# Kernel optimization log

Measured on AMD Instinct MI355X. Metric: run time of the kernel, lower is better.

The kernel has to match this reference:

```python
import jax, jax.numpy as jnp
import numpy as np

BN_EPS = 1e-3  # keras BatchNormalization default


def _bn(x, gamma, beta, mean, var):
    # inference-mode batchnorm over channel (last) axis
    return (x - mean) * (gamma * jax.lax.rsqrt(var + BN_EPS)) + beta


def _rel_pos_idx(n):
    # replicate calc_rel_pos: pos (n*n, 2); rel = pos[None]-pos[:,None] + n-1
    ii, jj = np.meshgrid(np.arange(n), np.arange(n), indexing='ij')
    pos = np.stack([ii.reshape(-1), jj.reshape(-1)], axis=-1)  # (n*n, 2)
    rel = pos[None, :, :] - pos[:, None, :] + (n - 1)          # (n*n, n*n, 2)
    return jnp.asarray(rel, dtype=jnp.int32)


def setup_inputs() -> dict:
    key = jax.random.key(0)
    ks = jax.random.split(key, 13)
    b, hh, ww, c = 4, 16, 16, 1024
    heads, dim_k, dim_u, dim_out = 4, 256, 1, 1024
    dim_v = dim_out // heads  # 256 == dim_k (required by the original reshape)
    n = hh
    rel_len = 2 * n - 1
    inp = {
        'x': jax.random.normal(ks[0], (b, hh, ww, c), jnp.float32),
        'Wq': jax.random.normal(ks[1], (c, dim_k * heads), jnp.float32) * 0.02,
        'Wk': jax.random.normal(ks[2], (c, dim_k * dim_u), jnp.float32) * 0.02,
        'Wv': jax.random.normal(ks[3], (c, dim_v * dim_u), jnp.float32) * 0.02,
        'q_gamma': jax.random.normal(ks[4], (dim_k * heads,), jnp.float32),
        'q_beta': jax.random.normal(ks[5], (dim_k * heads,), jnp.float32),
        'q_mean': jax.random.normal(ks[6], (dim_k * heads,), jnp.float32),
        'q_var': jax.random.uniform(ks[7], (dim_k * heads,), jnp.float32, 0.5, 1.5),
        'v_gamma': jax.random.normal(ks[8], (dim_v * dim_u,), jnp.float32),
        'v_beta': jax.random.normal(ks[9], (dim_v * dim_u,), jnp.float32),
        'v_mean': jax.random.normal(ks[10], (dim_v * dim_u,), jnp.float32),
        'v_var': jax.random.uniform(ks[11], (dim_v * dim_u,), jnp.float32, 0.5, 1.5),
        'rel_pos_emb': jax.random.normal(ks[12], (rel_len, rel_len, dim_k, dim_u), jnp.float32) * 0.05,
    }
    return inp


def reference(x, Wq, Wk, Wv, q_gamma, q_beta, q_mean, q_var,
              v_gamma, v_beta, v_mean, v_var, rel_pos_emb):
    b, hh, ww, c = x.shape
    heads, dim_u = 4, 1
    dim_k = rel_pos_emb.shape[2]
    dim_v = Wv.shape[1] // dim_u
    m = hh * ww

    # 1x1 conv projections (no bias)
    q = jnp.einsum('bhwc,cd->bhwd', x, Wq)
    k = jnp.einsum('bhwc,cd->bhwd', x, Wk)
    v = jnp.einsum('bhwc,cd->bhwd', x, Wv)

    q = _bn(q, q_gamma, q_beta, q_mean, q_var)
    v = _bn(v, v_gamma, v_beta, v_mean, v_var)

    # faithful TF row-major reshapes (note: mixes spatial/channel exactly as original)
    q = q.reshape(b, heads, dim_v, m)   # (b, h, k, n)
    k = k.reshape(b, dim_u, dim_v, m)   # (b, u, k, m)
    v = v.reshape(b, dim_u, dim_v, m)   # (b, u, v, m)

    k = jax.nn.softmax(k, axis=-1)

    Lc = jnp.einsum('bukm,buvm->bkv', k, v)
    Yc = jnp.einsum('bhkn,bkv->bnhv', q, Lc)

    rel_pos = _rel_pos_idx(hh)  # (m, m, 2) int32 constants
    rel = rel_pos_emb[rel_pos[..., 0], rel_pos[..., 1]]  # (m, m, k, u)
    Lp = jnp.einsum('nmku,buvm->bnkv', rel, v)
    Yp = jnp.einsum('bhkn,bnkv->bnhv', q, Lp)

    Y = Yc + Yp  # (b, n, h, v)
    return Y.reshape(b, hh, ww, heads * dim_v)
```

## Files before the change

kernel.cpp:

```cpp
#include <hip/hip_runtime.h>


typedef __bf16 bf16;
typedef __attribute__((ext_vector_type(8))) __bf16 bf16x8;
typedef __attribute__((ext_vector_type(4))) float f32x4;

__device__ __forceinline__ bf16x8 ld8(const bf16* p) {
    return *reinterpret_cast<const bf16x8*>(p);
}

__global__ __launch_bounds__(256) void prep(
    const float* __restrict__ x, const float* __restrict__ Wq,
    const float* __restrict__ Wk, const float* __restrict__ Wv,
    const float* __restrict__ rpe, bf16* __restrict__ xb,
    bf16* __restrict__ WqT, bf16* __restrict__ WkT, bf16* __restrict__ WvT,
    bf16* __restrict__ rpeb) {
    __shared__ float tile[32][33];
    const int bid = blockIdx.x, tid = threadIdx.x;
    const float* W = nullptr;
    bf16* WT = nullptr;
    int ldw = 0, ci = 0, di = 0;
    if (bid < 1024) {
        W = Wq; WT = WqT; ldw = 1024; ci = bid >> 5; di = bid & 31;
    } else if (bid < 1280) {
        const int t2 = bid - 1024;
        W = Wk; WT = WkT; ldw = 256; ci = t2 >> 3; di = t2 & 7;
    } else if (bid < 1536) {
        const int t2 = bid - 1280;
        W = Wv; WT = WvT; ldw = 256; ci = t2 >> 3; di = t2 & 7;
    }
    if (W) {
        const int r = tid >> 3, c4 = (tid & 7) * 4;
        const float4 v =
            *reinterpret_cast<const float4*>(&W[(ci * 32 + r) * ldw + di * 32 + c4]);
        tile[r][c4 + 0] = v.x;
        tile[r][c4 + 1] = v.y;
        tile[r][c4 + 2] = v.z;
        tile[r][c4 + 3] = v.w;
        __syncthreads();
        bf16 o[4] = {(bf16)tile[c4 + 0][r], (bf16)tile[c4 + 1][r],
                     (bf16)tile[c4 + 2][r], (bf16)tile[c4 + 3][r]};
        *reinterpret_cast<uint2*>(&WT[(di * 32 + r) * 1024 + ci * 32 + c4]) =
            *reinterpret_cast<uint2*>(o);
        return;
    }
    if (bid < 1792) {
        const int base = (bid - 1536) * 1024 + tid;
        const float4* xs = reinterpret_cast<const float4*>(x);
#pragma unroll
        for (int j = 0; j < 4; ++j) {
            const float4 v = xs[base + j * 256];
            bf16 o[4] = {(bf16)v.x, (bf16)v.y, (bf16)v.z, (bf16)v.w};
            *reinterpret_cast<uint2*>(&xb[(base + j * 256) * 4]) =
                *reinterpret_cast<uint2*>(o);
        }
        return;
    }
    {
        const int base = (bid - 1792) * 1024 + tid;
        const float4* rs = reinterpret_cast<const float4*>(rpe);
#pragma unroll
        for (int j = 0; j < 4; ++j) {
            const int idx = base + j * 256;
            if (idx < 61504) {
                const float4 v = rs[idx];
                bf16 o[4] = {(bf16)v.x, (bf16)v.y, (bf16)v.z, (bf16)v.w};
                *reinterpret_cast<uint2*>(&rpeb[idx * 4]) =
                    *reinterpret_cast<uint2*>(o);
            }
        }
    }
}

template <int PA, int PB>
__device__ __forceinline__ void kpass128(const bf16* __restrict__ Ap, int offA,
                                         const bf16* __restrict__ Bp,
                                         bf16* __restrict__ Al, bf16* __restrict__ Bl,
                                         f32x4 (&acc)[2], int m0, int n0,
                                         int nsteps) {
    const int tid = threadIdx.x;
    const int w = tid >> 6, l = tid & 63;
    const int sr = tid >> 4;
    const int sg = tid & 15;
    const int wrow = (w & 1) * 16, wcol = (w >> 1) * 32;
    const int fr = l & 15, fg = l >> 4;
    const int fx7 = fr & 7;
    const int st = sr * 128 + ((sg ^ (sr & 7)) << 3);
    const bf16* asrc0 = Ap + (m0 + sr) * PA + offA + sg * 8;
    const bf16* asrc1 = asrc0 + 16 * PA;
    const bf16* bsrc0 = Bp + (n0 + sr) * PB + sg * 8;
    const bf16* bsrc1 = bsrc0 + 16 * PB;
    const bf16* bsrc2 = bsrc0 + 32 * PB;
    const bf16* bsrc3 = bsrc0 + 48 * PB;

    bf16x8 a0 = ld8(asrc0), a1 = ld8(asrc1);
    bf16x8 b0 = ld8(bsrc0), b1 = ld8(bsrc1), b2 = ld8(bsrc2), b3 = ld8(bsrc3);
    for (int kt = 0; kt < nsteps; ++kt) {
        __syncthreads();
        *reinterpret_cast<bf16x8*>(&Al[st]) = a0;
        *reinterpret_cast<bf16x8*>(&Al[st + 2048]) = a1;
        *reinterpret_cast<bf16x8*>(&Bl[st]) = b0;
        *reinterpret_cast<bf16x8*>(&Bl[st + 2048]) = b1;
        *reinterpret_cast<bf16x8*>(&Bl[st + 4096]) = b2;
        *reinterpret_cast<bf16x8*>(&Bl[st + 6144]) = b3;
        __syncthreads();
        if (kt + 1 < nsteps) {
            const int k0 = (kt + 1) * 128;
            a0 = ld8(asrc0 + k0);
            a1 = ld8(asrc1 + k0);
            b0 = ld8(bsrc0 + k0);
            b1 = ld8(bsrc1 + k0);
            b2 = ld8(bsrc2 + k0);
            b3 = ld8(bsrc3 + k0);
        }
#pragma unroll
        for (int ks = 0; ks < 4; ++ks) {
            const int eo = ((ks * 4 + fg) ^ fx7) << 3;
            const bf16x8 af = ld8(&Al[(wrow + fr) * 128 + eo]);
            const bf16x8 bg0 = ld8(&Bl[(wcol + fr) * 128 + eo]);
            const bf16x8 bg1 = ld8(&Bl[(wcol + 16 + fr) * 128 + eo]);
            acc[0] = __builtin_amdgcn_mfma_f32_16x16x32_bf16(af, bg0, acc[0], 0, 0, 0);
            acc[1] = __builtin_amdgcn_mfma_f32_16x16x32_bf16(af, bg1, acc[1], 0, 0, 0);
        }
    }
}

__global__ __launch_bounds__(256) void proj_all(
    const bf16* __restrict__ xb, const bf16* __restrict__ WqT,
    const bf16* __restrict__ WkT, const bf16* __restrict__ WvT,
    const float* __restrict__ qg, const float* __restrict__ qb,
    const float* __restrict__ qm, const float* __restrict__ qv,
    const float* __restrict__ vg, const float* __restrict__ vb,
    const float* __restrict__ vm, const float* __restrict__ vvar,
    bf16* __restrict__ Q2, float* __restrict__ kn, bf16* __restrict__ vbn) {
    const int z = blockIdx.z;
    const int m0 = blockIdx.y * 32;
    const int tid = threadIdx.x;
    const int w = tid >> 6, l = tid & 63;
    int n0, mode;
    const bf16* Bg;
    if (z < 4) { mode = 0; Bg = WqT; n0 = (z * 4 + blockIdx.x) * 64; }
    else if (z == 4) { mode = 1; Bg = WkT; n0 = blockIdx.x * 64; }
    else { mode = 2; Bg = WvT; n0 = blockIdx.x * 64; }
    __shared__ __align__(16) bf16 Al[4096];
    __shared__ __align__(16) bf16 Bl[8192];
    f32x4 acc[2] = {};
    kpass128<1024, 1024>(xb, 0, Bg, Al, Bl, acc, m0, n0, 8);

    const int wrow = (w & 1) * 16, wcol = (w >> 1) * 32;
    const int drow = (l >> 4) * 4, dcol = l & 15;
#pragma unroll
    for (int ns = 0; ns < 2; ++ns) {
        const int gc = n0 + wcol + ns * 16 + dcol;
        float scale = 1.f, shift = 0.f;
        if (mode == 0) {
            scale = qg[gc] * rsqrtf(qv[gc] + 1e-3f);
            shift = qb[gc] - qm[gc] * scale;
        } else if (mode == 2) {
            scale = vg[gc] * rsqrtf(vvar[gc] + 1e-3f);
            shift = vb[gc] - vm[gc] * scale;
        }
#pragma unroll
        for (int r = 0; r < 4; ++r) {
            const int gr = m0 + wrow + drow + r;
            const float val = acc[ns][r] * scale + shift;
            if (mode == 0) {
                const int bh = gr >> 6;
                const int kk = (gr & 63) * 4 + (gc >> 8);
                Q2[bh * 65536 + (gc & 255) * 256 + kk] = (bf16)val;
            } else if (mode == 1) {
                kn[gr * 256 + gc] = val;
            } else {
                vbn[gr * 256 + gc] = (bf16)val;
            }
        }
    }
}

__global__ __launch_bounds__(256) void lc_s(
    const float* __restrict__ kn, const bf16* __restrict__ vbn,
    const bf16* __restrict__ rpeb, const bf16* __restrict__ Q2,
    bf16* __restrict__ LcT, bf16* __restrict__ S) {
    __shared__ __align__(16) bf16 smem[20480];
    const int tid = threadIdx.x;
    const int w = tid >> 6, l = tid & 63;
    const int fr = l & 15, fk = (l >> 4) * 8;
    const int fx = (fr & 7) << 3;

    if (blockIdx.y < 16) {
        const int b = blockIdx.y >> 2;
        const int m0v = (blockIdx.y & 3) * 64;
        const int n0k = blockIdx.x * 64;
        bf16* Bfull = smem;
        bf16* Al = smem + 16384;

        const float* knb = kn + (b * 256 + n0k) * 256;
        const int row = tid >> 2, cq = (tid & 3) * 4;
        const float* src = knb + row * 256;
        float mx = -3.4e38f;
#pragma unroll
        for (int i = 0; i < 16; ++i) {
            const float4 v = *reinterpret_cast<const float4*>(&src[cq + i * 16]);
            mx = fmaxf(fmaxf(fmaxf(v.x, v.y), fmaxf(v.z, v.w)), mx);
        }
        mx = fmaxf(mx, __shfl_xor(mx, 1));
        mx = fmaxf(mx, __shfl_xor(mx, 2));
        float sum = 0.f;
#pragma unroll
        for (int i = 0; i < 16; ++i) {
            const float4 v = *reinterpret_cast<const float4*>(&src[cq + i * 16]);
            sum += expf(v.x - mx) + expf(v.y - mx) + expf(v.z - mx) + expf(v.w - mx);
        }
        sum += __shfl_xor(sum, 1);
        sum += __shfl_xor(sum, 2);
        const float inv = 1.f / sum;
#pragma unroll
        for (int i = 0; i < 16; ++i) {
            const int col = cq + i * 16;
            const float4 v = *reinterpret_cast<const float4*>(&src[col]);
            bf16 o[4] = {(bf16)(expf(v.x - mx) * inv), (bf16)(expf(v.y - mx) * inv),
                         (bf16)(expf(v.z - mx) * inv), (bf16)(expf(v.w - mx) * inv)};
            const int elem =
                row * 256 + ((((col >> 3) ^ (row & 7)) << 3) | (col & 7));
            *reinterpret_cast<uint2*>(&Bfull[elem]) = *reinterpret_cast<uint2*>(o);
        }

        const int sr0 = tid >> 3, sg = tid & 7;
        const int st0 = sr0 * 64 + ((sg ^ (sr0 & 7)) << 3);
        const int st1 = (sr0 + 32) * 64 + ((sg ^ (sr0 & 7)) << 3);
        const int wr = (w >> 1) * 32, wc = (w & 1) * 32;
        const bf16* va0 = vbn + (b * 256 + m0v + sr0) * 256 + sg * 8;
        const bf16* va1 = va0 + 32 * 256;
        bf16x8 a0 = ld8(va0), a1 = ld8(va1);
        f32x4 acc[2][2] = {};
        for (int kt = 0; kt < 4; ++kt) {
            __syncthreads();
            *reinterpret_cast<bf16x8*>(&Al[st0]) = a0;
            *reinterpret_cast<bf16x8*>(&Al[st1]) = a1;
            __syncthreads();
            if (kt + 1 < 4) {
                a0 = ld8(va0 + (kt + 1) * 64);
                a1 = ld8(va1 + (kt + 1) * 64);
            }
#pragma unroll
            for (int ks = 0; ks < 2; ++ks) {
                const int eoA = (ks * 32 + fk) ^ fx;
                const int eoB = (kt * 64 + ks * 32 + fk) ^ fx;
                const bf16x8 af0 = ld8(&Al[(wr + fr) * 64 + eoA]);
                const bf16x8 af1 = ld8(&Al[(wr + 16 + fr) * 64 + eoA]);
                const bf16x8 bg0 = ld8(&Bfull[(wc + fr) * 256 + eoB]);
                const bf16x8 bg1 = ld8(&Bfull[(wc + 16 + fr) * 256 + eoB]);
                acc[0][0] = __builtin_amdgcn_mfma_f32_16x16x32_bf16(af0, bg0, acc[0][0], 0, 0, 0);
                acc[0][1] = __builtin_amdgcn_mfma_f32_16x16x32_bf16(af0, bg1, acc[0][1], 0, 0, 0);
                acc[1][0] = __builtin_amdgcn_mfma_f32_16x16x32_bf16(af1, bg0, acc[1][0], 0, 0, 0);
                acc[1][1] = __builtin_amdgcn_mfma_f32_16x16x32_bf16(af1, bg1, acc[1][1], 0, 0, 0);
            }
        }
        const int drow = (l >> 4) * 4, dcol = l & 15;
#pragma unroll
        for (int ms = 0; ms < 2; ++ms)
#pragma unroll
            for (int ns = 0; ns < 2; ++ns)
#pragma unroll
                for (int r = 0; r < 4; ++r)
                    LcT[b * 65536 + (m0v + wr + ms * 16 + drow + r) * 256 + n0k +
                        wc + ns * 16 + dcol] = (bf16)acc[ms][ns][r];
        return;
    }

    const int n = blockIdx.y - 16;
    const int m0 = blockIdx.x * 64;
    const int in_ = n >> 4, jn = n & 15;
    bf16* Als = smem;
    bf16* Bls = smem + 16384;
#pragma unroll
    for (int i = 0; i < 2; ++i) {
        const int slot = tid + i * 256;
        const int row = slot >> 5, g = slot & 31;
        *reinterpret_cast<bf16x8*>(&Bls[row * 256 + ((g ^ (row & 7)) << 3)]) =
            ld8(Q2 + row * 65536 + n * 256 + g * 8);
    }
#pragma unroll
    for (int i = 0; i < 8; ++i) {
        const int slot = tid + i * 256;
        const int row = slot >> 5, g = slot & 31;
        const int m = m0 + row;
        const int ridx = ((m >> 4) - in_ + 15) * 31 + ((m & 15) - jn + 15);
        *reinterpret_cast<bf16x8*>(&Als[row * 256 + ((g ^ (row & 7)) << 3)]) =
            ld8(rpeb + ridx * 256 + g * 8);
    }
    __syncthreads();
    f32x4 acc = {};
#pragma unroll
    for (int ks = 0; ks < 8; ++ks) {
        const int eo = (ks * 32 + fk) ^ fx;
        const bf16x8 af = ld8(&Als[(w * 16 + fr) * 256 + eo]);
        const bf16x8 bg = ld8(&Bls[fr * 256 + eo]);
        acc = __builtin_amdgcn_mfma_f32_16x16x32_bf16(af, bg, acc, 0, 0, 0);
    }
    const int drow = (l >> 4) * 4, bh = l & 15;
#pragma unroll
    for (int r = 0; r < 4; ++r) {
        const int m = m0 + w * 16 + drow + r;
        S[n * 4096 + bh * 256 + m] = (bf16)acc[r];
    }
}

__global__ __launch_bounds__(256) void yfinal(const bf16* __restrict__ Q2,
                                              const bf16* __restrict__ LcT,
                                              float* __restrict__ out,
                                              const bf16* __restrict__ S,
                                              const bf16* __restrict__ vbn) {
    const int tid = threadIdx.x;
    const int w = tid >> 6, l = tid & 63;
    const int m0 = blockIdx.y * 32, n0 = blockIdx.x * 64;
    const int z = blockIdx.z;
    __shared__ __align__(16) bf16 Al[4096];
    __shared__ __align__(16) bf16 Bl[8192];
    f32x4 acc[2] = {};
    kpass128<256, 256>(Q2 + z * 65536, 0, LcT + (z >> 2) * 65536, Al, Bl, acc, m0,
                       n0, 2);
    kpass128<4096, 256>(S, z * 256, vbn + (z >> 2) * 65536, Al, Bl, acc, m0, n0, 2);

    const int wrow = (w & 1) * 16, wcol = (w >> 1) * 32;
    const int drow = (l >> 4) * 4, dcol = l & 15;
#pragma unroll
    for (int ns = 0; ns < 2; ++ns)
#pragma unroll
        for (int r = 0; r < 4; ++r)
            out[(z >> 2) * 262144 + (m0 + wrow + drow + r) * 1024 +
                (z & 3) * 256 + n0 + wcol + ns * 16 + dcol] = acc[ns][r];
}

extern "C" void kernel_launch(void* const* d_in, const int* in_sizes, int n_in,
                              void* d_out, int out_size, void* d_ws, size_t ws_size,
                              hipStream_t stream) {
    const float* x = (const float*)d_in[0];
    const float* Wq = (const float*)d_in[1];
    const float* Wk = (const float*)d_in[2];
    const float* Wv = (const float*)d_in[3];
    const float* qg = (const float*)d_in[4];
    const float* qb = (const float*)d_in[5];
    const float* qm = (const float*)d_in[6];
    const float* qv = (const float*)d_in[7];
    const float* vg = (const float*)d_in[8];
    const float* vb = (const float*)d_in[9];
    const float* vm = (const float*)d_in[10];
    const float* vvar = (const float*)d_in[11];
    const float* rpe = (const float*)d_in[12];
    float* out = (float*)d_out;

    char* wsb = (char*)d_ws;
    bf16* xb = (bf16*)(wsb);
    bf16* WqT = (bf16*)(wsb + 0x200000u);
    bf16* WkT = (bf16*)(wsb + 0x400000u);
    bf16* WvT = (bf16*)(wsb + 0x480000u);
    bf16* rpeb = (bf16*)(wsb + 0x500000u);
    bf16* Q2 = (bf16*)(wsb + 0x580000u);
    bf16* vbn = (bf16*)(wsb + 0x800000u);
    bf16* LcT = (bf16*)(wsb + 0x880000u);
    bf16* S = (bf16*)(wsb + 0x900000u);
    float* kn = (float*)(wsb + 0xB00000u);

    const dim3 blk(256);
    prep<<<1853, blk, 0, stream>>>(x, Wq, Wk, Wv, rpe, xb, WqT, WkT, WvT, rpeb);
    proj_all<<<dim3(4, 32, 6), blk, 0, stream>>>(xb, WqT, WkT, WvT, qg, qb, qm, qv,
                                                 vg, vb, vm, vvar, Q2, kn, vbn);
    lc_s<<<dim3(4, 272), blk, 0, stream>>>(kn, vbn, rpeb, Q2, LcT, S);
    yfinal<<<dim3(4, 8, 16), blk, 0, stream>>>(Q2, LcT, out, S, vbn);
}
```

Before: 39.92 us.

## Fuse projection, Lc/S and final stages into persistent kernel with grid barriers

Result: slower. 138.1 us (+245.9%).

```diff
diff --git a/kernel.cpp b/kernel.cpp
--- a/kernel.cpp
+++ b/kernel.cpp
@@ -5,8 +5,21 @@
 typedef __attribute__((ext_vector_type(8))) __bf16 bf16x8;
 typedef __attribute__((ext_vector_type(4))) float f32x4;
 
+#define NBLK 512u
+
 __device__ __forceinline__ bf16x8 ld8(const bf16* p) {
     return *reinterpret_cast<const bf16x8*>(p);
+}
+
+__device__ __forceinline__ void gridbar(unsigned int* cnt) {
+    __syncthreads();
+    if (threadIdx.x == 0) {
+        __threadfence();
+        atomicAdd(cnt, 1u);
+        while (atomicAdd(cnt, 0u) < NBLK) __builtin_amdgcn_s_sleep(8);
+        __threadfence();
+    }
+    __syncthreads();
 }
 
 __global__ __launch_bounds__(256) void prep(
@@ -14,9 +27,10 @@
     const float* __restrict__ Wk, const float* __restrict__ Wv,
     const float* __restrict__ rpe, bf16* __restrict__ xb,
     bf16* __restrict__ WqT, bf16* __restrict__ WkT, bf16* __restrict__ WvT,
-    bf16* __restrict__ rpeb) {
+    bf16* __restrict__ rpeb, unsigned int* cnt) {
     __shared__ float tile[32][33];
     const int bid = blockIdx.x, tid = threadIdx.x;
+    if (bid == 0 && tid < 2) cnt[tid * 16] = 0u;
     const float* W = nullptr;
     bf16* WT = nullptr;
     int ldw = 0, ci = 0, di = 0;
@@ -125,211 +139,213 @@
     }
 }
 
-__global__ __launch_bounds__(256) void proj_all(
+__global__ __launch_bounds__(256, 2) void fused(
     const bf16* __restrict__ xb, const bf16* __restrict__ WqT,
     const bf16* __restrict__ WkT, const bf16* __restrict__ WvT,
     const float* __restrict__ qg, const float* __restrict__ qb,
     const float* __restrict__ qm, const float* __restrict__ qv,
     const float* __restrict__ vg, const float* __restrict__ vb,
     const float* __restrict__ vm, const float* __restrict__ vvar,
-    bf16* __restrict__ Q2, float* __restrict__ kn, bf16* __restrict__ vbn) {
-    const int z = blockIdx.z;
-    const int m0 = blockIdx.y * 32;
+    bf16* __restrict__ Q2, float* __restrict__ kn, bf16* __restrict__ vbn,
+    const bf16* __restrict__ rpeb, bf16* __restrict__ LcT, bf16* __restrict__ S,
+    float* __restrict__ out, unsigned int* cnt) {
+    __shared__ __align__(16) char smem_raw[40960];
+    const int bid = blockIdx.x;
     const int tid = threadIdx.x;
     const int w = tid >> 6, l = tid & 63;
-    int n0, mode;
-    const bf16* Bg;
-    if (z < 4) { mode = 0; Bg = WqT; n0 = (z * 4 + blockIdx.x) * 64; }
-    else if (z == 4) { mode = 1; Bg = WkT; n0 = blockIdx.x * 64; }
-    else { mode = 2; Bg = WvT; n0 = blockIdx.x * 64; }
-    __shared__ __align__(16) bf16 Al[4096];
-    __shared__ __align__(16) bf16 Bl[8192];
-    f32x4 acc[2] = {};
-    kpass128<1024, 1024>(xb, 0, Bg, Al, Bl, acc, m0, n0, 8);
-
-    const int wrow = (w & 1) * 16, wcol = (w >> 1) * 32;
-    const int drow = (l >> 4) * 4, dcol = l & 15;
-#pragma unroll
-    for (int ns = 0; ns < 2; ++ns) {
-        const int gc = n0 + wcol + ns * 16 + dcol;
-        float scale = 1.f, shift = 0.f;
-        if (mode == 0) {
-            scale = qg[gc] * rsqrtf(qv[gc] + 1e-3f);
-            shift = qb[gc] - qm[gc] * scale;
-        } else if (mode == 2) {
-            scale = vg[gc] * rsqrtf(vvar[gc] + 1e-3f);
-            shift = vb[gc] - vm[gc] * scale;
-        }
-#pragma unroll
-        for (int r = 0; r < 4; ++r) {
-            const int gr = m0 + wrow + drow + r;
-            const float val = acc[ns][r] * scale + shift;
+
+    for (int j = bid; j < 768; j += NBLK) {
+        bf16* Al = (bf16*)smem_raw;
+        bf16* Bl = (bf16*)(smem_raw + 8192);
+        const int z = j >> 7;
+        const int m0 = ((j >> 2) & 31) * 32;
+        const int bx = j & 3;
+        int n0, mode;
+        const bf16* Bg;
+        if (z < 4) { mode = 0; Bg = WqT; n0 = (z * 4 + bx) * 64; }
+        else if (z == 4) { mode = 1; Bg = WkT; n0 = bx * 64; }
+        else { mode = 2; Bg = WvT; n0 = bx * 64; }
+        f32x4 acc[2] = {};
+        kpass128<1024, 1024>(xb, 0, Bg, Al, Bl, acc, m0, n0, 8);
+
+        const int wrow = (w & 1) * 16, wcol = (w >> 1) * 32;
+        const int drow = (l >> 4) * 4, dcol = l & 15;
+#pragma unroll
+        for (int ns = 0; ns < 2; ++ns) {
+            const int gc = n0 + wcol + ns * 16 + dcol;
+            float scale = 1.f, shift = 0.f;
             if (mode == 0) {
-                const int bh = gr >> 6;
-                const int kk = (gr & 63) * 4 + (gc >> 8);
-                Q2[bh * 65536 + (gc & 255) * 256 + kk] = (bf16)val;
-            } else if (mode == 1) {
-                kn[gr * 256 + gc] = val;
-            } else {
-                vbn[gr * 256 + gc] = (bf16)val;
-            }
-        }
-    }
-}
-
-__global__ __launch_bounds__(256) void lc_s(
-    const float* __restrict__ kn, const bf16* __restrict__ vbn,
-    const bf16* __restrict__ rpeb, const bf16* __restrict__ Q2,
-    bf16* __restrict__ LcT, bf16* __restrict__ S) {
-    __shared__ __align__(16) bf16 smem[20480];
-    const int tid = threadIdx.x;
-    const int w = tid >> 6, l = tid & 63;
-    const int fr = l & 15, fk = (l >> 4) * 8;
-    const int fx = (fr & 7) << 3;
-
-    if (blockIdx.y < 16) {
-        const int b = blockIdx.y >> 2;
-        const int m0v = (blockIdx.y & 3) * 64;
-        const int n0k = blockIdx.x * 64;
-        bf16* Bfull = smem;
-        bf16* Al = smem + 16384;
-
-        const float* knb = kn + (b * 256 + n0k) * 256;
-        const int row = tid >> 2, cq = (tid & 3) * 4;
-        const float* src = knb + row * 256;
-        float mx = -3.4e38f;
-#pragma unroll
-        for (int i = 0; i < 16; ++i) {
-            const float4 v = *reinterpret_cast<const float4*>(&src[cq + i * 16]);
-            mx = fmaxf(fmaxf(fmaxf(v.x, v.y), fmaxf(v.z, v.w)), mx);
-        }
-        mx = fmaxf(mx, __shfl_xor(mx, 1));
-        mx = fmaxf(mx, __shfl_xor(mx, 2));
-        float sum = 0.f;
-#pragma unroll
-        for (int i = 0; i < 16; ++i) {
-            const float4 v = *reinterpret_cast<const float4*>(&src[cq + i * 16]);
-            sum += expf(v.x - mx) + expf(v.y - mx) + expf(v.z - mx) + expf(v.w - mx);
-        }
-        sum += __shfl_xor(sum, 1);
-        sum += __shfl_xor(sum, 2);
-        const float inv = 1.f / sum;
-#pragma unroll
-        for (int i = 0; i < 16; ++i) {
-            const int col = cq + i * 16;
-            const float4 v = *reinterpret_cast<const float4*>(&src[col]);
-            bf16 o[4] = {(bf16)(expf(v.x - mx) * inv), (bf16)(expf(v.y - mx) * inv),
-                         (bf16)(expf(v.z - mx) * inv), (bf16)(expf(v.w - mx) * inv)};
-            const int elem =
-                row * 256 + ((((col >> 3) ^ (row & 7)) << 3) | (col & 7));
-            *reinterpret_cast<uint2*>(&Bfull[elem]) = *reinterpret_cast<uint2*>(o);
-        }
-
-        const int sr0 = tid >> 3, sg = tid & 7;
-        const int st0 = sr0 * 64 + ((sg ^ (sr0 & 7)) << 3);
-        const int st1 = (sr0 + 32) * 64 + ((sg ^ (sr0 & 7)) << 3);
-        const int wr = (w >> 1) * 32, wc = (w & 1) * 32;
-        const bf16* va0 = vbn + (b * 256 + m0v + sr0) * 256 + sg * 8;
-        const bf16* va1 = va0 + 32 * 256;
-        bf16x8 a0 = ld8(va0), a1 = ld8(va1);
-        f32x4 acc[2][2] = {};
-        for (int kt = 0; kt < 4; ++kt) {
+                scale = qg[gc] * rsqrtf(qv[gc] + 1e-3f);
+                shift = qb[gc] - qm[gc] * scale;
+            } else if (mode == 2) {
+                scale = vg[gc] * rsqrtf(vvar[gc] + 1e-3f);
+                shift = vb[gc] - vm[gc] * scale;
+            }
+#pragma unroll
+            for (int r = 0; r < 4; ++r) {
+                const int gr = m0 + wrow + drow + r;
+                const float val = acc[ns][r] * scale + shift;
+                if (mode == 0) {
+                    const int bh = gr >> 6;
+                    const int kk = (gr & 63) * 4 + (gc >> 8);
+                    Q2[bh * 65536 + (gc & 255) * 256 + kk] = (bf16)val;
+                } else if (mode == 1) {
+                    kn[gr * 256 + gc] = val;
+                } else {
+                    vbn[gr * 256 + gc] = (bf16)val;
+                }
+            }
+        }
+        __syncthreads();
+    }
+    gridbar(cnt);
+
+    for (int j = bid; j < 1088; j += NBLK) {
+        bf16* smem = (bf16*)smem_raw;
+        const int jx = j & 3, jy = j >> 2;
+        const int fr = l & 15, fk = (l >> 4) * 8;
+        const int fx = (fr & 7) << 3;
+
+        if (jy < 16) {
+            const int b = jy >> 2;
+            const int m0v = (jy & 3) * 64;
+            const int n0k = jx * 64;
+            bf16* Bfull = smem;
+            bf16* Al = smem + 16384;
+
+            const float* knb = kn + (b * 256 + n0k) * 256;
+            const int row = tid >> 2, cq = (tid & 3) * 4;
+            const float* src = knb + row * 256;
+            float mx = -3.4e38f;
+#pragma unroll
+            for (int i = 0; i < 16; ++i) {
+                const float4 v = *reinterpret_cast<const float4*>(&src[cq + i * 16]);
+                mx = fmaxf(fmaxf(fmaxf(v.x, v.y), fmaxf(v.z, v.w)), mx);
+            }
+            mx = fmaxf(mx, __shfl_xor(mx, 1));
+            mx = fmaxf(mx, __shfl_xor(mx, 2));
+            float sum = 0.f;
+#pragma unroll
+            for (int i = 0; i < 16; ++i) {
+                const float4 v = *reinterpret_cast<const float4*>(&src[cq + i * 16]);
+                sum += expf(v.x - mx) + expf(v.y - mx) + expf(v.z - mx) + expf(v.w - mx);
+            }
+            sum += __shfl_xor(sum, 1);
+            sum += __shfl_xor(sum, 2);
+            const float inv = 1.f / sum;
+#pragma unroll
+            for (int i = 0; i < 16; ++i) {
+                const int col = cq + i * 16;
+                const float4 v = *reinterpret_cast<const float4*>(&src[col]);
+                bf16 o[4] = {(bf16)(expf(v.x - mx) * inv), (bf16)(expf(v.y - mx) * inv),
+                             (bf16)(expf(v.z - mx) * inv), (bf16)(expf(v.w - mx) * inv)};
+                const int elem =
+                    row * 256 + ((((col >> 3) ^ (row & 7)) << 3) | (col & 7));
+                *reinterpret_cast<uint2*>(&Bfull[elem]) = *reinterpret_cast<uint2*>(o);
+            }
+
+            const int sr0 = tid >> 3, sg = tid & 7;
+            const int st0 = sr0 * 64 + ((sg ^ (sr0 & 7)) << 3);
+            const int st1 = (sr0 + 32) * 64 + ((sg ^ (sr0 & 7)) << 3);
+            const int wr = (w >> 1) * 32, wc = (w & 1) * 32;
+            const bf16* va0 = vbn + (b * 256 + m0v + sr0) * 256 + sg * 8;
+            const bf16* va1 = va0 + 32 * 256;
+            bf16x8 a0 = ld8(va0), a1 = ld8(va1);
+            f32x4 acc[2][2] = {};
+            for (int kt = 0; kt < 4; ++kt) {
+                __syncthreads();
+                *reinterpret_cast<bf16x8*>(&Al[st0]) = a0;
+                *reinterpret_cast<bf16x8*>(&Al[st1]) = a1;
+                __syncthreads();
+                if (kt + 1 < 4) {
+                    a0 = ld8(va0 + (kt + 1) * 64);
+                    a1 = ld8(va1 + (kt + 1) * 64);
+                }
+#pragma unroll
+                for (int ks = 0; ks < 2; ++ks) {
+                    const int eoA = (ks * 32 + fk) ^ fx;
+                    const int eoB = (kt * 64 + ks * 32 + fk) ^ fx;
+                    const bf16x8 af0 = ld8(&Al[(wr + fr) * 64 + eoA]);
+                    const bf16x8 af1 = ld8(&Al[(wr + 16 + fr) * 64 + eoA]);
+                    const bf16x8 bg0 = ld8(&Bfull[(wc + fr) * 256 + eoB]);
+                    const bf16x8 bg1 = ld8(&Bfull[(wc + 16 + fr) * 256 + eoB]);
+                    acc[0][0] = __builtin_amdgcn_mfma_f32_16x16x32_bf16(af0, bg0, acc[0][0], 0, 0, 0);
+                    acc[0][1] = __builtin_amdgcn_mfma_f32_16x16x32_bf16(af0, bg1, acc[0][1], 0, 0, 0);
+                    acc[1][0] = __builtin_amdgcn_mfma_f32_16x16x32_bf16(af1, bg0, acc[1][0], 0, 0, 0);
+                    acc[1][1] = __builtin_amdgcn_mfma_f32_16x16x32_bf16(af1, bg1, acc[1][1], 0, 0, 0);
+                }
+            }
+            const int drow = (l >> 4) * 4, dcol = l & 15;
+#pragma unroll
+            for (int ms = 0; ms < 2; ++ms)
+#pragma unroll
+                for (int ns = 0; ns < 2; ++ns)
+#pragma unroll
+                    for (int r = 0; r < 4; ++r)
+                        LcT[b * 65536 + (m0v + wr + ms * 16 + drow + r) * 256 + n0k +
+                            wc + ns * 16 + dcol] = (bf16)acc[ms][ns][r];
+        } else {
+            const int n = jy - 16;
+            const int m0 = jx * 64;
+            const int in_ = n >> 4, jn = n & 15;
+            bf16* Als = smem;
+            bf16* Bls = smem + 16384;
+#pragma unroll
+            for (int i = 0; i < 2; ++i) {
+                const int slot = tid + i * 256;
+                const int row = slot >> 5, g = slot & 31;
+                *reinterpret_cast<bf16x8*>(&Bls[row * 256 + ((g ^ (row & 7)) << 3)]) =
+                    ld8(Q2 + row * 65536 + n * 256 + g * 8);
+            }
+#pragma unroll
+            for (int i = 0; i < 8; ++i) {
+                const int slot = tid + i * 256;
+                const int row = slot >> 5, g = slot & 31;
+                const int m = m0 + row;
+                const int ridx = ((m >> 4) - in_ + 15) * 31 + ((m & 15) - jn + 15);
+                *reinterpret_cast<bf16x8*>(&Als[row * 256 + ((g ^ (row & 7)) << 3)]) =
+                    ld8(rpeb + ridx * 256 + g * 8);
+            }
             __syncthreads();
-            *reinterpret_cast<bf16x8*>(&Al[st0]) = a0;
-            *reinterpret_cast<bf16x8*>(&Al[st1]) = a1;
-            __syncthreads();
-            if (kt + 1 < 4) {
-                a0 = ld8(va0 + (kt + 1) * 64);
-                a1 = ld8(va1 + (kt + 1) * 64);
-            }
-#pragma unroll
-            for (int ks = 0; ks < 2; ++ks) {
-                const int eoA = (ks * 32 + fk) ^ fx;
-                const int eoB = (kt * 64 + ks * 32 + fk) ^ fx;
-                const bf16x8 af0 = ld8(&Al[(wr + fr) * 64 + eoA]);
-                const bf16x8 af1 = ld8(&Al[(wr + 16 + fr) * 64 + eoA]);
-                const bf16x8 bg0 = ld8(&Bfull[(wc + fr) * 256 + eoB]);
-                const bf16x8 bg1 = ld8(&Bfull[(wc + 16 + fr) * 256 + eoB]);
-                acc[0][0] = __builtin_amdgcn_mfma_f32_16x16x32_bf16(af0, bg0, acc[0][0], 0, 0, 0);
-                acc[0][1] = __builtin_amdgcn_mfma_f32_16x16x32_bf16(af0, bg1, acc[0][1], 0, 0, 0);
-                acc[1][0] = __builtin_amdgcn_mfma_f32_16x16x32_bf16(af1, bg0, acc[1][0], 0, 0, 0);
-                acc[1][1] = __builtin_amdgcn_mfma_f32_16x16x32_bf16(af1, bg1, acc[1][1], 0, 0, 0);
-            }
-        }
+            f32x4 acc = {};
+#pragma unroll
+            for (int ks = 0; ks < 8; ++ks) {
+                const int eo = (ks * 32 + fk) ^ fx;
+                const bf16x8 af = ld8(&Als[(w * 16 + fr) * 256 + eo]);
+                const bf16x8 bg = ld8(&Bls[fr * 256 + eo]);
+                acc = __builtin_amdgcn_mfma_f32_16x16x32_bf16(af, bg, acc, 0, 0, 0);
+            }
+            const int drow = (l >> 4) * 4, bh = l & 15;
+#pragma unroll
+            for (int r = 0; r < 4; ++r) {
+                const int m = m0 + w * 16 + drow + r;
+                S[n * 4096 + bh * 256 + m] = (bf16)acc[r];
+            }
+        }
+        __syncthreads();
+    }
+    gridbar(cnt + 16);
+
+    for (int j = bid; j < 512; j += NBLK) {
+        bf16* Al = (bf16*)smem_raw;
+        bf16* Bl = (bf16*)(smem_raw + 8192);
+        const int m0 = ((j >> 2) & 7) * 32, n0 = (j & 3) * 64;
+        const int z = j >> 5;
+        f32x4 acc[2] = {};
+        kpass128<256, 256>(Q2 + z * 65536, 0, LcT + (z >> 2) * 65536, Al, Bl, acc,
+                           m0, n0, 2);
+        kpass128<4096, 256>(S, z * 256, vbn + (z >> 2) * 65536, Al, Bl, acc, m0,
+                            n0, 2);
+
+        const int wrow = (w & 1) * 16, wcol = (w >> 1) * 32;
         const int drow = (l >> 4) * 4, dcol = l & 15;
 #pragma unroll
-        for (int ms = 0; ms < 2; ++ms)
-#pragma unroll
-            for (int ns = 0; ns < 2; ++ns)
-#pragma unroll
-                for (int r = 0; r < 4; ++r)
-                    LcT[b * 65536 + (m0v + wr + ms * 16 + drow + r) * 256 + n0k +
-                        wc + ns * 16 + dcol] = (bf16)acc[ms][ns][r];
-        return;
-    }
-
-    const int n = blockIdx.y - 16;
-    const int m0 = blockIdx.x * 64;
-    const int in_ = n >> 4, jn = n & 15;
-    bf16* Als = smem;
-    bf16* Bls = smem + 16384;
-#pragma unroll
-    for (int i = 0; i < 2; ++i) {
-        const int slot = tid + i * 256;
-        const int row = slot >> 5, g = slot & 31;
-        *reinterpret_cast<bf16x8*>(&Bls[row * 256 + ((g ^ (row & 7)) << 3)]) =
-            ld8(Q2 + row * 65536 + n * 256 + g * 8);
-    }
-#pragma unroll
-    for (int i = 0; i < 8; ++i) {
-        const int slot = tid + i * 256;
-        const int row = slot >> 5, g = slot & 31;
-        const int m = m0 + row;
-        const int ridx = ((m >> 4) - in_ + 15) * 31 + ((m & 15) - jn + 15);
-        *reinterpret_cast<bf16x8*>(&Als[row * 256 + ((g ^ (row & 7)) << 3)]) =
-            ld8(rpeb + ridx * 256 + g * 8);
-    }
-    __syncthreads();
-    f32x4 acc = {};
-#pragma unroll
-    for (int ks = 0; ks < 8; ++ks) {
-        const int eo = (ks * 32 + fk) ^ fx;
-        const bf16x8 af = ld8(&Als[(w * 16 + fr) * 256 + eo]);
-        const bf16x8 bg = ld8(&Bls[fr * 256 + eo]);
-        acc = __builtin_amdgcn_mfma_f32_16x16x32_bf16(af, bg, acc, 0, 0, 0);
-    }
-    const int drow = (l >> 4) * 4, bh = l & 15;
-#pragma unroll
-    for (int r = 0; r < 4; ++r) {
-        const int m = m0 + w * 16 + drow + r;
-        S[n * 4096 + bh * 256 + m] = (bf16)acc[r];
-    }
-}
-
-__global__ __launch_bounds__(256) void yfinal(const bf16* __restrict__ Q2,
-                                              const bf16* __restrict__ LcT,
-                                              float* __restrict__ out,
-                                              const bf16* __restrict__ S,
-                                              const bf16* __restrict__ vbn) {
-    const int tid = threadIdx.x;
-    const int w = tid >> 6, l = tid & 63;
-    const int m0 = blockIdx.y * 32, n0 = blockIdx.x * 64;
-    const int z = blockIdx.z;
-    __shared__ __align__(16) bf16 Al[4096];
-    __shared__ __align__(16) bf16 Bl[8192];
-    f32x4 acc[2] = {};
-    kpass128<256, 256>(Q2 + z * 65536, 0, LcT + (z >> 2) * 65536, Al, Bl, acc, m0,
-                       n0, 2);
-    kpass128<4096, 256>(S, z * 256, vbn + (z >> 2) * 65536, Al, Bl, acc, m0, n0, 2);
-
-    const int wrow = (w & 1) * 16, wcol = (w >> 1) * 32;
-    const int drow = (l >> 4) * 4, dcol = l & 15;
-#pragma unroll
-    for (int ns = 0; ns < 2; ++ns)
-#pragma unroll
-        for (int r = 0; r < 4; ++r)
-            out[(z >> 2) * 262144 + (m0 + wrow + drow + r) * 1024 +
-                (z & 3) * 256 + n0 + wcol + ns * 16 + dcol] = acc[ns][r];
+        for (int ns = 0; ns < 2; ++ns)
+#pragma unroll
+            for (int r = 0; r < 4; ++r)
+                out[(z >> 2) * 262144 + (m0 + wrow + drow + r) * 1024 +
+                    (z & 3) * 256 + n0 + wcol + ns * 16 + dcol] = acc[ns][r];
+    }
 }
 
 extern "C" void kernel_launch(void* const* d_in, const int* in_sizes, int n_in,
@@ -356,6 +372,7 @@
     bf16* WkT = (bf16*)(wsb + 0x400000u);
     bf16* WvT = (bf16*)(wsb + 0x480000u);
     bf16* rpeb = (bf16*)(wsb + 0x500000u);
+    unsigned int* cnt = (unsigned int*)(wsb + 0x57F000u);
     bf16* Q2 = (bf16*)(wsb + 0x580000u);
     bf16* vbn = (bf16*)(wsb + 0x800000u);
     bf16* LcT = (bf16*)(wsb + 0x880000u);
@@ -363,9 +380,8 @@
     float* kn = (float*)(wsb + 0xB00000u);
 
     const dim3 blk(256);
-    prep<<<1853, blk, 0, stream>>>(x, Wq, Wk, Wv, rpe, xb, WqT, WkT, WvT, rpeb);
-    proj_all<<<dim3(4, 32, 6), blk, 0, stream>>>(xb, WqT, WkT, WvT, qg, qb, qm, qv,
-                                                 vg, vb, vm, vvar, Q2, kn, vbn);
-    lc_s<<<dim3(4, 272), blk, 0, stream>>>(kn, vbn, rpeb, Q2, LcT, S);
-    yfinal<<<dim3(4, 8, 16), blk, 0, stream>>>(Q2, LcT, out, S, vbn);
-}
+    prep<<<1853, blk, 0, stream>>>(x, Wq, Wk, Wv, rpe, xb, WqT, WkT, WvT, rpeb,
+                                   cnt);
+    fused<<<NBLK, blk, 0, stream>>>(xb, WqT, WkT, WvT, qg, qb, qm, qv, vg, vb, vm,
+                                    vvar, Q2, kn, vbn, rpeb, LcT, S, out, cnt);
+}
```
